# Performance work log

Measured on AMD Instinct MI355X. Metric: run time of the kernel, lower is better.

## Reference

```python
import jax, jax.numpy as jnp
import numpy as np

B, n, D, L, Hff, heads = 64, 512, 128, 3, 512, 8
N = B * n
deg = 16
E = N * deg
dh = D // heads
EPS = 1e-5


def setup_inputs() -> dict:
    key = jax.random.key(0)
    ks = jax.random.split(key, 16)
    x = jax.random.normal(ks[0], (N, D), jnp.float32)
    # within-graph random edges (TSP kNN-style), offset per graph
    src = jax.random.randint(ks[1], (B, n * deg), 0, n)
    dst = jax.random.randint(ks[2], (B, n * deg), 0, n)
    off = (jnp.arange(B) * n)[:, None]
    edge_index = jnp.stack([(src + off).reshape(-1), (dst + off).reshape(-1)]).astype(jnp.int32)
    edge_attr = jax.random.normal(ks[3], (E, D), jnp.float32)
    batch = jnp.repeat(jnp.arange(B, dtype=jnp.int32), n)
    s = 0.02
    wk = jax.random.split(ks[4], 8)
    w = lambda k, shape: jax.random.normal(k, shape, jnp.float32) * s
    return dict(
        x=x, edge_index=edge_index, edge_attr=edge_attr, batch=batch,
        Wq=w(wk[0], (L, D, D)), bq=jnp.zeros((L, D), jnp.float32),
        Wk=w(wk[1], (L, D, D)), bk=jnp.zeros((L, D), jnp.float32),
        Wv=w(wk[2], (L, D, D)), bv=jnp.zeros((L, D), jnp.float32),
        We=w(wk[3], (L, D, D)),  # lin_edge has no bias in PyG TransformerConv
        Wskip=w(wk[4], (L, D, D)), bskip=jnp.zeros((L, D), jnp.float32),
        gn_g=jnp.ones((L - 1, D), jnp.float32), gn_b=jnp.zeros((L - 1, D), jnp.float32),
        gn_a=jnp.ones((L - 1, D), jnp.float32),
        ffW1=w(wk[5], (D, Hff)), ffb1=jnp.zeros((Hff,), jnp.float32),
        fgn_g=jnp.ones((Hff,), jnp.float32), fgn_b=jnp.zeros((Hff,), jnp.float32),
        fgn_a=jnp.ones((Hff,), jnp.float32),
        ffW2=w(wk[6], (Hff, D)), ffb2=jnp.zeros((D,), jnp.float32),
    )


def _graph_norm(x, batch, gamma, beta, alpha):
    # GraphNorm: per-graph mean/var per channel, learnable mean scale alpha
    mean = jax.ops.segment_sum(x, batch, num_segments=B) / n
    xc = x - alpha * mean[batch]
    var = jax.ops.segment_sum(xc * xc, batch, num_segments=B) / n
    return gamma * xc * jax.lax.rsqrt(var[batch] + EPS) + beta


def _transformer_conv(x, src, dst, ea, Wq, bq, Wk, bk, Wv, bv, We, Ws, bs):
    q = (x @ Wq + bq).reshape(-1, heads, dh)
    k = (x @ Wk + bk).reshape(-1, heads, dh)
    v = (x @ Wv + bv).reshape(-1, heads, dh)
    e = (ea @ We).reshape(-1, heads, dh)
    ke = k[src] + e                                   # [E, h, dh]
    score = jnp.einsum('ehd,ehd->eh', q[dst], ke) / np.sqrt(dh)
    m = jax.ops.segment_max(score, dst, num_segments=N)
    ex = jnp.exp(score - m[dst])
    denom = jax.ops.segment_sum(ex, dst, num_segments=N)
    alpha = ex / denom[dst]                           # softmax over in-neighbors
    msg = alpha[..., None] * (v[src] + e)
    out = jax.ops.segment_sum(msg, dst, num_segments=N).reshape(-1, D)
    return out + x @ Ws + bs                          # root/skip connection


def reference(x, edge_index, edge_attr, batch, Wq, bq, Wk, bk, Wv, bv, We, Wskip, bskip,
              gn_g, gn_b, gn_a, ffW1, ffb1, fgn_g, fgn_b, fgn_a, ffW2, ffb2):
    src, dst = edge_index[0], edge_index[1]
    for i in range(L):
        x = _transformer_conv(x, src, dst, edge_attr, Wq[i], bq[i], Wk[i], bk[i],
                              Wv[i], bv[i], We[i], Wskip[i], bskip[i])
        if i < L - 1:
            x = _graph_norm(jax.nn.gelu(x, approximate=False), batch, gn_g[i], gn_b[i], gn_a[i])
        else:
            h = jax.nn.gelu(x @ ffW1 + ffb1, approximate=False)
            h = _graph_norm(h, batch, fgn_g, fgn_b, fgn_a)
            x = h @ ffW2 + ffb2
    node_embeddings = x.reshape(B, n, D)
    graph_feat = jax.ops.segment_sum(x, batch, num_segments=B) / n  # mean pool
    return node_embeddings, graph_feat
```

## Files before the change

### kernel.cpp

```cpp
#include <hip/hip_runtime.h>
#include <hip/hip_bf16.h>
#include <math.h>

typedef unsigned short u16;
typedef __attribute__((ext_vector_type(4))) float floatx4;
typedef __attribute__((ext_vector_type(8))) short shortx8;

#define NB 64
#define NNODE 512
#define NTOT (NB*NNODE)
#define DDIM 128
#define DEG 16
#define NEDGE (NTOT*DEG)
#define HFF 512
#define EPSV 1e-5f
#define BFRAG_U16 16384
#define EPI_LD 136

__device__ __forceinline__ float bf2f(u16 u){
  union { unsigned int i; float f; } v; v.i = ((unsigned int)u) << 16; return v.f;
}
__device__ __forceinline__ u16 f2bf(float f){
  union { float f; unsigned int i; } v; v.f = f;
  unsigned int r = v.i + 0x7FFFu + ((v.i >> 16) & 1u);
  return (u16)(r >> 16);
}
__device__ __forceinline__ float gelu_f(float x){
  return 0.5f * x * (1.0f + erff(x * 0.70710678118654752f));
}

__global__ void prep_kernel(const float* __restrict__ x, u16* __restrict__ xb,
                            int* __restrict__ counts, float* __restrict__ pool){
  int gid = blockIdx.x*256 + threadIdx.x;
  if (gid < NTOT) counts[gid] = 0;
  if (gid < NB*DDIM) pool[gid] = 0.f;
  int i = gid*4;
  float4 f = *(const float4*)(x + i);
  ushort4 o; o.x = f2bf(f.x); o.y = f2bf(f.y); o.z = f2bf(f.z); o.w = f2bf(f.w);
  *(ushort4*)(xb + i) = o;
}

__global__ void hist_kernel(const int* __restrict__ dst, int* __restrict__ counts){
  int e = blockIdx.x*256 + threadIdx.x; atomicAdd(&counts[dst[e]], 1);
}
__global__ void scan_kernel(const int* counts, int* row_ptr, int* cursor){
  __shared__ int part[1024];
  int t = threadIdx.x; int base = t*32;
  int loc[32]; int s = 0;
  #pragma unroll
  for (int i = 0; i < 32; ++i){ loc[i] = counts[base+i]; s += loc[i]; }
  part[t] = s; __syncthreads();
  for (int off = 1; off < 1024; off <<= 1){
    int v = (t >= off) ? part[t-off] : 0;
    __syncthreads(); part[t] += v; __syncthreads();
  }
  int run = part[t] - s;
  #pragma unroll
  for (int i = 0; i < 32; ++i){ row_ptr[base+i] = run; cursor[base+i] = run; run += loc[i]; }
  if (t == 0) row_ptr[NTOT] = part[1023];
}
__global__ void scatter_kernel(const int* __restrict__ src, const int* __restrict__ dst,
                               int* __restrict__ cursor, int* __restrict__ ssrc, int* __restrict__ seid){
  int e = blockIdx.x*256 + threadIdx.x;
  int d = dst[e];
  int pos = atomicAdd(&cursor[d], 1);
  ssrc[pos] = src[e]; seid[pos] = e;
}

__global__ __launch_bounds__(512, 2)
void egemm3_kernel(const float* __restrict__ ea, const int* __restrict__ seid,
                   const float* __restrict__ We, u16* __restrict__ eout, int niter){
  __shared__ u16 bfrag[3*BFRAG_U16];
  __shared__ u16 epi_s[8*16*EPI_LD];
  const int t = threadIdx.x;
  const int wave = t >> 6, lane = t & 63, quad = lane >> 4, l16 = lane & 15;
  for (int p = wave; p < 12; p += 8){
    const int l = p >> 2, kk = p & 3;
    const float* Bp = We + (size_t)l*DDIM*DDIM;
    #pragma unroll
    for (int nt = 0; nt < 8; ++nt){
      int colB = nt*16 + l16;
      shortx8 pk;
      #pragma unroll
      for (int j = 0; j < 8; ++j)
        pk[j] = (short)f2bf(Bp[(size_t)(kk*32 + quad*8 + j)*DDIM + colB]);
      *(shortx8*)&bfrag[((size_t)l*2048 + (kk*8 + nt)*64 + lane)*8] = pk;
    }
  }
  __syncthreads();
  u16* epi = &epi_s[wave*16*EPI_LD];
  for (int it = blockIdx.x; it < niter; it += gridDim.x){
    const int wrow0 = it*256 + wave*32;
    const int r0 = wrow0 + l16, r1 = r0 + 16;
    const long ar0 = (long)seid[r0], ar1 = (long)seid[r1];
    shortx8 af[2][4];
    #pragma unroll
    for (int kk = 0; kk < 4; ++kk){
      float4 x0 = *(const float4*)(ea + ar0*DDIM + kk*32 + quad*8);
      float4 x1 = *(const float4*)(ea + ar0*DDIM + kk*32 + quad*8 + 4);
      float4 y0 = *(const float4*)(ea + ar1*DDIM + kk*32 + quad*8);
      float4 y1 = *(const float4*)(ea + ar1*DDIM + kk*32 + quad*8 + 4);
      shortx8 a0, a1;
      a0[0]=(short)f2bf(x0.x); a0[1]=(short)f2bf(x0.y); a0[2]=(short)f2bf(x0.z); a0[3]=(short)f2bf(x0.w);
      a0[4]=(short)f2bf(x1.x); a0[5]=(short)f2bf(x1.y); a0[6]=(short)f2bf(x1.z); a0[7]=(short)f2bf(x1.w);
      a1[0]=(short)f2bf(y0.x); a1[1]=(short)f2bf(y0.y); a1[2]=(short)f2bf(y0.z); a1[3]=(short)f2bf(y0.w);
      a1[4]=(short)f2bf(y1.x); a1[5]=(short)f2bf(y1.y); a1[6]=(short)f2bf(y1.z); a1[7]=(short)f2bf(y1.w);
      af[0][kk] = a0; af[1][kk] = a1;
    }
    #pragma unroll
    for (int l = 0; l < 3; ++l){
      floatx4 acc[2][8] = {};
      #pragma unroll
      for (int kk = 0; kk < 4; ++kk){
        #pragma unroll
        for (int nt = 0; nt < 8; ++nt){
          shortx8 bfr = *(const shortx8*)&bfrag[((size_t)l*2048 + (kk*8 + nt)*64 + lane)*8];
          acc[0][nt] = __builtin_amdgcn_mfma_f32_16x16x32_bf16(af[0][kk], bfr, acc[0][nt], 0, 0, 0);
          acc[1][nt] = __builtin_amdgcn_mfma_f32_16x16x32_bf16(af[1][kk], bfr, acc[1][nt], 0, 0, 0);
        }
      }
      u16* o16 = eout + (size_t)l*NEDGE*DDIM;
      #pragma unroll
      for (int mt = 0; mt < 2; ++mt){
        #pragma unroll
        for (int nt = 0; nt < 8; ++nt){
          #pragma unroll
          for (int r = 0; r < 4; ++r)
            epi[(quad*4 + r)*EPI_LD + nt*16 + l16] = f2bf(acc[mt][nt][r]);
        }
        #pragma unroll
        for (int j = 0; j < 4; ++j){
          int row = j*4 + quad;
          uint4 d = *(const uint4*)&epi[row*EPI_LD + l16*8];
          *(uint4*)(o16 + (size_t)(wrow0 + mt*16 + row)*DDIM + l16*8) = d;
        }
      }
    }
  }
}

struct Gemm2Cfg {
  const float* B[4];
  const float* bias[4];
  float* o32[4];
  u16* o16[4];
  const int* a_idx;
  const float* nA;
  const float* nBp;
  int ldb, ld_out, bcolmul, ocolmul, gelu, mtiles;
};

template<bool ABF>
__global__ __launch_bounds__(256, 3)
void gemm2_kernel(const void* __restrict__ Aptr, Gemm2Cfg cfg){
  __shared__ u16 lds[BFRAG_U16 + 4*16*EPI_LD];
  const int t = threadIdx.x;
  const int wave = t >> 6, lane = t & 63, quad = lane >> 4, l16 = lane & 15;
  const int cb = blockIdx.y;
  const float* Bp = cfg.B[cb];
  const int col0b = cb * cfg.bcolmul;
  {
    const int kk = wave;
    #pragma unroll
    for (int nt = 0; nt < 8; ++nt){
      int colB = col0b + nt*16 + l16;
      shortx8 pk;
      #pragma unroll
      for (int j = 0; j < 8; ++j)
        pk[j] = (short)f2bf(Bp[(size_t)(kk*32 + quad*8 + j)*cfg.ldb + colB]);
      *(shortx8*)&lds[((kk*8 + nt)*64 + lane)*8] = pk;
    }
  }
  __syncthreads();
  const float* biasp = cfg.bias[cb];
  const int col0o = cb * cfg.ocolmul;
  float bias_r[8];
  #pragma unroll
  for (int nt = 0; nt < 8; ++nt)
    bias_r[nt] = biasp ? biasp[col0o + nt*16 + l16] : 0.0f;
  u16* epi = &lds[BFRAG_U16 + wave*16*EPI_LD];

  for (int tile = blockIdx.x; tile < cfg.mtiles; tile += gridDim.x){
    const int wrow0 = tile*128 + wave*32;
    const int r0 = wrow0 + l16, r1 = wrow0 + 16 + l16;
    const long ar0 = cfg.a_idx ? (long)cfg.a_idx[r0] : (long)r0;
    const long ar1 = cfg.a_idx ? (long)cfg.a_idx[r1] : (long)r1;
    shortx8 af[2][4];
    if (ABF){
      const u16* Ab = (const u16*)Aptr;
      #pragma unroll
      for (int kk = 0; kk < 4; ++kk){
        af[0][kk] = *(const shortx8*)(Ab + ar0*128 + kk*32 + quad*8);
        af[1][kk] = *(const shortx8*)(Ab + ar1*128 + kk*32 + quad*8);
      }
    } else {
      const float* Af = (const float*)Aptr;
      const int g = wrow0 >> 9;
      #pragma unroll
      for (int kk = 0; kk < 4; ++kk){
        float4 x0 = *(const float4*)(Af + ar0*128 + kk*32 + quad*8);
        float4 x1 = *(const float4*)(Af + ar0*128 + kk*32 + quad*8 + 4);
        float4 y0 = *(const float4*)(Af + ar1*128 + kk*32 + quad*8);
        float4 y1 = *(const float4*)(Af + ar1*128 + kk*32 + quad*8 + 4);
        if (cfg.nA){
          const float4 A0 = *(const float4*)(cfg.nA  + (size_t)g*DDIM + kk*32 + quad*8);
          const float4 A1 = *(const float4*)(cfg.nA  + (size_t)g*DDIM + kk*32 + quad*8 + 4);
          const float4 B0 = *(const float4*)(cfg.nBp + (size_t)g*DDIM + kk*32 + quad*8);
          const float4 B1 = *(const float4*)(cfg.nBp + (size_t)g*DDIM + kk*32 + quad*8 + 4);
          x0.x = gelu_f(x0.x)*A0.x + B0.x; x0.y = gelu_f(x0.y)*A0.y + B0.y;
          x0.z = gelu_f(x0.z)*A0.z + B0.z; x0.w = gelu_f(x0.w)*A0.w + B0.w;
          x1.x = gelu_f(x1.x)*A1.x + B1.x; x1.y = gelu_f(x1.y)*A1.y + B1.y;
          x1.z = gelu_f(x1.z)*A1.z + B1.z; x1.w = gelu_f(x1.w)*A1.w + B1.w;
          y0.x = gelu_f(y0.x)*A0.x + B0.x; y0.y = gelu_f(y0.y)*A0.y + B0.y;
          y0.z = gelu_f(y0.z)*A0.z + B0.z; y0.w = gelu_f(y0.w)*A0.w + B0.w;
          y1.x = gelu_f(y1.x)*A1.x + B1.x; y1.y = gelu_f(y1.y)*A1.y + B1.y;
          y1.z = gelu_f(y1.z)*A1.z + B1.z; y1.w = gelu_f(y1.w)*A1.w + B1.w;
        }
        shortx8 a0, a1;
        a0[0]=(short)f2bf(x0.x); a0[1]=(short)f2bf(x0.y); a0[2]=(short)f2bf(x0.z); a0[3]=(short)f2bf(x0.w);
        a0[4]=(short)f2bf(x1.x); a0[5]=(short)f2bf(x1.y); a0[6]=(short)f2bf(x1.z); a0[7]=(short)f2bf(x1.w);
        a1[0]=(short)f2bf(y0.x); a1[1]=(short)f2bf(y0.y); a1[2]=(short)f2bf(y0.z); a1[3]=(short)f2bf(y0.w);
        a1[4]=(short)f2bf(y1.x); a1[5]=(short)f2bf(y1.y); a1[6]=(short)f2bf(y1.z); a1[7]=(short)f2bf(y1.w);
        af[0][kk] = a0; af[1][kk] = a1;
      }
    }
    floatx4 acc[2][8] = {};
    #pragma unroll
    for (int kk = 0; kk < 4; ++kk){
      #pragma unroll
      for (int nt = 0; nt < 8; ++nt){
        shortx8 bfr = *(const shortx8*)&lds[((kk*8 + nt)*64 + lane)*8];
        acc[0][nt] = __builtin_amdgcn_mfma_f32_16x16x32_bf16(af[0][kk], bfr, acc[0][nt], 0, 0, 0);
        acc[1][nt] = __builtin_amdgcn_mfma_f32_16x16x32_bf16(af[1][kk], bfr, acc[1][nt], 0, 0, 0);
      }
    }
    u16* o16 = cfg.o16[cb];
    if (o16){
      #pragma unroll
      for (int mt = 0; mt < 2; ++mt){
        #pragma unroll
        for (int nt = 0; nt < 8; ++nt){
          #pragma unroll
          for (int r = 0; r < 4; ++r){
            float v = acc[mt][nt][r] + bias_r[nt];
            if (cfg.gelu) v = gelu_f(v);
            epi[(quad*4 + r)*EPI_LD + nt*16 + l16] = f2bf(v);
          }
        }
        #pragma unroll
        for (int j = 0; j < 4; ++j){
          int row = j*4 + quad;
          uint4 d = *(const uint4*)&epi[row*EPI_LD + l16*8];
          *(uint4*)(o16 + (size_t)(wrow0 + mt*16 + row)*cfg.ld_out + col0o + l16*8) = d;
        }
      }
    } else {
      float* o32 = cfg.o32[cb];
      #pragma unroll
      for (int nt = 0; nt < 8; ++nt){
        #pragma unroll
        for (int mt = 0; mt < 2; ++mt){
          #pragma unroll
          for (int r = 0; r < 4; ++r){
            int row = wrow0 + mt*16 + quad*4 + r;
            float v = acc[mt][nt][r] + bias_r[nt];
            if (cfg.gelu) v = gelu_f(v);
            o32[(size_t)row*cfg.ld_out + col0o + nt*16 + l16] = v;
          }
        }
      }
    }
  }
}

struct GemmCfg {
  const float* B[4];
  const float* bias[4];
  float* o32[4];
  u16* o16[4];
  float* pool;
  const float* nA;
  const float* nBp;
  int ldb, ld_out, K, bcolmul, ocolmul, gelu;
};

__global__ __launch_bounds__(256, 2)
void gemm_old(const u16* __restrict__ Ab, GemmCfg cfg){
  __shared__ u16 As[128][136];
  __shared__ u16 Bs[128][136];
  const int t = threadIdx.x;
  const int wave = t >> 6, lane = t & 63, quad = lane >> 4, l16 = lane & 15;
  const int row0 = blockIdx.x * 128;
  const int cb = blockIdx.y;
  const float* Bp = cfg.B[cb];
  const int col0b = cb * cfg.bcolmul;
  const int K = cfg.K;
  const int g = row0 >> 9;
  floatx4 acc[2][8] = {};
  for (int kc = 0; kc < K; kc += 128){
    #pragma unroll
    for (int j = 0; j < 8; ++j){
      int idx8 = t + j*256;
      int elem = idx8 << 3;
      int r = elem >> 7, c = elem & 127;
      uint4 d = *(const uint4*)(Ab + (size_t)(row0+r)*K + kc + c);
      if (cfg.nA){
        const float4 A0 = *(const float4*)(cfg.nA  + (size_t)g*K + kc + c);
        const float4 A1 = *(const float4*)(cfg.nA  + (size_t)g*K + kc + c + 4);
        const float4 B0 = *(const float4*)(cfg.nBp + (size_t)g*K + kc + c);
        const float4 B1 = *(const float4*)(cfg.nBp + (size_t)g*K + kc + c + 4);
        u16* pu = (u16*)&d;
        pu[0] = f2bf(bf2f(pu[0])*A0.x + B0.x);
        pu[1] = f2bf(bf2f(pu[1])*A0.y + B0.y);
        pu[2] = f2bf(bf2f(pu[2])*A0.z + B0.z);
        pu[3] = f2bf(bf2f(pu[3])*A0.w + B0.w);
        pu[4] = f2bf(bf2f(pu[4])*A1.x + B1.x);
        pu[5] = f2bf(bf2f(pu[5])*A1.y + B1.y);
        pu[6] = f2bf(bf2f(pu[6])*A1.z + B1.z);
        pu[7] = f2bf(bf2f(pu[7])*A1.w + B1.w);
      }
      *(uint4*)&As[r][c] = d;
    }
    #pragma unroll
    for (int j = 0; j < 16; ++j){
      int gi = t + j*256;
      int c = gi & 127;
      int k4 = (gi >> 7) << 2;
      size_t boff = (size_t)(kc + k4)*cfg.ldb + col0b + c;
      float f0 = Bp[boff];
      float f1 = Bp[boff + cfg.ldb];
      float f2 = Bp[boff + 2*(size_t)cfg.ldb];
      float f3 = Bp[boff + 3*(size_t)cfg.ldb];
      u16* wp = &Bs[c][k4];
      wp[0]=f2bf(f0); wp[1]=f2bf(f1); wp[2]=f2bf(f2); wp[3]=f2bf(f3);
    }
    __syncthreads();
    const int wm0 = wave*32;
    #pragma unroll
    for (int kk = 0; kk < 4; ++kk){
      shortx8 a0 = *(const shortx8*)&As[wm0 + l16][kk*32 + quad*8];
      shortx8 a1 = *(const shortx8*)&As[wm0 + 16 + l16][kk*32 + quad*8];
      #pragma unroll
      for (int nt = 0; nt < 8; ++nt){
        shortx8 bfr = *(const shortx8*)&Bs[nt*16 + l16][kk*32 + quad*8];
        acc[0][nt] = __builtin_amdgcn_mfma_f32_16x16x32_bf16(a0, bfr, acc[0][nt], 0, 0, 0);
        acc[1][nt] = __builtin_amdgcn_mfma_f32_16x16x32_bf16(a1, bfr, acc[1][nt], 0, 0, 0);
      }
    }
    __syncthreads();
  }
  const float* biasp = cfg.bias[cb];
  float* o32 = cfg.o32[cb];
  const int col0o = cb * cfg.ocolmul;
  const int wm0 = wave*32;
  float* psum = (float*)As;
  if (cfg.pool){
    __syncthreads();
    if (t < 128) psum[t] = 0.f;
    __syncthreads();
  }
  #pragma unroll
  for (int nt = 0; nt < 8; ++nt){
    int col = col0o + nt*16 + l16;
    float bvv = biasp ? biasp[col] : 0.0f;
    float cs = 0.f;
    #pragma unroll
    for (int mt = 0; mt < 2; ++mt){
      #pragma unroll
      for (int r = 0; r < 4; ++r){
        int row = row0 + wm0 + mt*16 + quad*4 + r;
        float v = acc[mt][nt][r] + bvv;
        if (cfg.gelu) v = gelu_f(v);
        o32[(size_t)row * cfg.ld_out + col] = v;
        cs += v;
      }
    }
    if (cfg.pool) atomicAdd(&psum[nt*16 + l16], cs);
  }
  if (cfg.pool){
    __syncthreads();
    if (t < 128) atomicAdd(&cfg.pool[(row0 >> 9)*DDIM + t], psum[t] * (1.0f/NNODE));
  }
}

__global__ __launch_bounds__(256)
void attn_kernel(const int* __restrict__ row_ptr, const int* __restrict__ ssrc,
                 const u16* __restrict__ e_rows,
                 const u16* __restrict__ qb, const u16* __restrict__ kb, const u16* __restrict__ vb,
                 const float* __restrict__ skip, float* __restrict__ y){
  int b = blockIdx.x;
  int xcd = b & 7, i = b >> 3;
  int g = xcd*8 + (i >> 7), slot = i & 127;
  int wave = threadIdx.x >> 6, lane = threadIdx.x & 63;
  int dst = g*NNODE + slot*4 + wave;
  const int ch = lane*2;
  ushort2 qp = *(const ushort2*)(qb + (size_t)dst*DDIM + ch);
  float q0 = bf2f(qp.x), q1 = bf2f(qp.y);
  int beg = row_ptr[dst], end = row_ptr[dst+1];
  float mh = -INFINITY, lh = 0.f, a0 = 0.f, a1 = 0.f;
  if (beg < end){
    int s = ssrc[beg];
    ushort2 ep = *(const ushort2*)(e_rows + (size_t)beg*DDIM + ch);
    ushort2 kp = *(const ushort2*)(kb + (size_t)s*DDIM + ch);
    ushort2 vp = *(const ushort2*)(vb + (size_t)s*DDIM + ch);
    for (int idx = beg; idx < end; ++idx){
      int nx = idx + 1;
      ushort2 epn = ep, kpn = kp, vpn = vp;
      if (nx < end){
        int sn = ssrc[nx];
        epn = *(const ushort2*)(e_rows + (size_t)nx*DDIM + ch);
        kpn = *(const ushort2*)(kb + (size_t)sn*DDIM + ch);
        vpn = *(const ushort2*)(vb + (size_t)sn*DDIM + ch);
      }
      float e0 = bf2f(ep.x), e1 = bf2f(ep.y);
      float p = q0*(bf2f(kp.x)+e0) + q1*(bf2f(kp.y)+e1);
      p += __shfl_xor(p, 1);
      p += __shfl_xor(p, 2);
      p += __shfl_xor(p, 4);
      float sc = p * 0.25f;
      float mn = fmaxf(mh, sc);
      float cs = __expf(mh - mn), w = __expf(sc - mn);
      lh = lh*cs + w;
      a0 = a0*cs + w*(bf2f(vp.x)+e0);
      a1 = a1*cs + w*(bf2f(vp.y)+e1);
      mh = mn;
      ep = epn; kp = kpn; vp = vpn;
    }
  }
  float r = lh > 0.f ? 1.0f/lh : 0.f;
  float2 sp = *(const float2*)(skip + (size_t)dst*DDIM + ch);
  float2 o; o.x = a0*r + sp.x; o.y = a1*r + sp.y;
  *(float2*)(y + (size_t)dst*DDIM + ch) = o;
}

__global__ __launch_bounds__(128)
void gstats_part(const float* __restrict__ y, float* __restrict__ ps, float* __restrict__ pq){
  int b = blockIdx.x, g = b >> 3, chunk = b & 7, c = threadIdx.x;
  const float* base = y + (size_t)g*NNODE*DDIM + (size_t)chunk*64*DDIM;
  float s = 0.f, q = 0.f;
  for (int i = 0; i < 64; ++i){
    float v = gelu_f(base[(size_t)i*DDIM + c]);
    s += v; q += v*v;
  }
  ps[b*DDIM + c] = s; pq[b*DDIM + c] = q;
}
__global__ __launch_bounds__(128)
void gstats_comb(const float* __restrict__ ps, const float* __restrict__ pq,
                 const float* __restrict__ gamma, const float* __restrict__ beta,
                 const float* __restrict__ alpha, float* __restrict__ nA, float* __restrict__ nB){
  int g = blockIdx.x, c = threadIdx.x;
  float s = 0.f, q = 0.f;
  #pragma unroll
  for (int j = 0; j < 8; ++j){ s += ps[(g*8+j)*DDIM + c]; q += pq[(g*8+j)*DDIM + c]; }
  float mean = s * (1.f/NNODE);
  float msq  = q * (1.f/NNODE);
  float a = alpha[c];
  float invv = rsqrtf(msq - mean*mean*a*(2.f-a) + EPSV);
  float ga = gamma[c]*invv;
  nA[g*DDIM + c] = ga;
  nB[g*DDIM + c] = beta[c] - ga*a*mean;
}

__global__ __launch_bounds__(512)
void fstats_part(const u16* __restrict__ gb, float* __restrict__ ps, float* __restrict__ pq){
  int b = blockIdx.x, g = b >> 3, chunk = b & 7, c = threadIdx.x;
  const u16* base = gb + (size_t)g*NNODE*HFF + (size_t)chunk*64*HFF;
  float s = 0.f, q = 0.f;
  for (int i = 0; i < 64; ++i){
    float v = bf2f(base[(size_t)i*HFF + c]);
    s += v; q += v*v;
  }
  ps[b*HFF + c] = s; pq[b*HFF + c] = q;
}
__global__ __launch_bounds__(512)
void fstats_comb(const float* __restrict__ ps, const float* __restrict__ pq,
                 const float* __restrict__ gamma, const float* __restrict__ beta,
                 const float* __restrict__ alpha, float* __restrict__ nA, float* __restrict__ nB){
  int g = blockIdx.x, c = threadIdx.x;
  float s = 0.f, q = 0.f;
  #pragma unroll
  for (int j = 0; j < 8; ++j){ s += ps[(g*8+j)*HFF + c]; q += pq[(g*8+j)*HFF + c]; }
  float mean = s * (1.f/NNODE);
  float msq  = q * (1.f/NNODE);
  float a = alpha[c];
  float invv = rsqrtf(msq - mean*mean*a*(2.f-a) + EPSV);
  float ga = gamma[c]*invv;
  nA[g*HFF + c] = ga;
  nB[g*HFF + c] = beta[c] - ga*a*mean;
}

extern "C" void kernel_launch(void* const* d_in, const int* in_sizes, int n_in,
                              void* d_out, int out_size, void* d_ws, size_t ws_size,
                              hipStream_t stream){
  const float* x_in = (const float*)d_in[0];
  const int*   eidx = (const int*)d_in[1];
  const float* ea   = (const float*)d_in[2];
  const float* Wq   = (const float*)d_in[4];
  const float* bq   = (const float*)d_in[5];
  const float* Wk   = (const float*)d_in[6];
  const float* bk   = (const float*)d_in[7];
  const float* Wv   = (const float*)d_in[8];
  const float* bv   = (const float*)d_in[9];
  const float* We   = (const float*)d_in[10];
  const float* Wsk  = (const float*)d_in[11];
  const float* bsk  = (const float*)d_in[12];
  const float* gn_g = (const float*)d_in[13];
  const float* gn_b = (const float*)d_in[14];
  const float* gn_a = (const float*)d_in[15];
  const float* ffW1 = (const float*)d_in[16];
  const float* ffb1 = (const float*)d_in[17];
  const float* fgn_g= (const float*)d_in[18];
  const float* fgn_b= (const float*)d_in[19];
  const float* fgn_a= (const float*)d_in[20];
  const float* ffW2 = (const float*)d_in[21];
  const float* ffb2 = (const float*)d_in[22];
  const int* srcA = eidx;
  const int* dstA = eidx + NEDGE;

  char* w = (char*)d_ws;
  auto alloc = [&](size_t bytes)->char*{ char* p = w; w += (bytes + 255) & ~(size_t)255; return p; };
  int* counts  = (int*)alloc((size_t)NTOT*4);
  int* row_ptr = (int*)alloc((size_t)(NTOT+1)*4);
  int* ssrc    = (int*)alloc((size_t)NEDGE*4);
  int* seid    = (int*)alloc((size_t)NEDGE*4);
  u16* e_bf    = (u16*)alloc((size_t)3*NEDGE*DDIM*2);
  u16* x_bf    = (u16*)alloc((size_t)NTOT*DDIM*2);
  u16* qb      = (u16*)alloc((size_t)NTOT*DDIM*2);
  u16* kb      = (u16*)alloc((size_t)NTOT*DDIM*2);
  u16* vb      = (u16*)alloc((size_t)NTOT*DDIM*2);
  float* skipb = (float*)alloc((size_t)NTOT*DDIM*4);
  float* yb    = (float*)alloc((size_t)NTOT*DDIM*4);
  float* nAb   = (float*)alloc((size_t)NB*HFF*4);
  float* nBb   = (float*)alloc((size_t)NB*HFF*4);
  float* psbuf = (float*)alloc((size_t)NB*8*HFF*4);
  float* pqbuf = (float*)alloc((size_t)NB*8*HFF*4);
  u16* g_bf  = e_bf;
  float* pool = (float*)d_out + (size_t)NTOT*DDIM;

  prep_kernel<<<NTOT*DDIM/1024, 256, 0, stream>>>(x_in, x_bf, counts, pool);
  hist_kernel<<<NEDGE/256, 256, 0, stream>>>(dstA, counts);
  scan_kernel<<<1, 1024, 0, stream>>>(counts, row_ptr, counts);
  scatter_kernel<<<NEDGE/256, 256, 0, stream>>>(srcA, dstA, counts, ssrc, seid);

  egemm3_kernel<<<512, 512, 0, stream>>>(ea, seid, We, e_bf, NEDGE/256);

  for (int l = 0; l < 3; ++l){
    Gemm2Cfg cq = {};
    cq.B[0]=Wq + (size_t)l*DDIM*DDIM; cq.B[1]=Wk + (size_t)l*DDIM*DDIM;
    cq.B[2]=Wv + (size_t)l*DDIM*DDIM; cq.B[3]=Wsk + (size_t)l*DDIM*DDIM;
    cq.bias[0]=bq + l*DDIM; cq.bias[1]=bk + l*DDIM; cq.bias[2]=bv + l*DDIM; cq.bias[3]=bsk + l*DDIM;
    cq.o16[0]=qb; cq.o16[1]=kb; cq.o16[2]=vb; cq.o16[3]=nullptr;
    cq.o32[3]=skipb;
    cq.ldb = DDIM; cq.ld_out = DDIM; cq.bcolmul = 0; cq.ocolmul = 0; cq.gelu = 0;
    cq.mtiles = NTOT/128;
    if (l == 0){
      gemm2_kernel<true><<<dim3(NTOT/128, 4), 256, 0, stream>>>(x_bf, cq);
    } else {
      cq.nA = nAb; cq.nBp = nBb;
      gemm2_kernel<false><<<dim3(NTOT/128, 4), 256, 0, stream>>>(yb, cq);
    }

    attn_kernel<<<NTOT/4, 256, 0, stream>>>(row_ptr, ssrc,
        e_bf + (size_t)l*NEDGE*DDIM, qb, kb, vb, skipb, yb);

    if (l < 2){
      gstats_part<<<NB*8, 128, 0, stream>>>(yb, psbuf, pqbuf);
      gstats_comb<<<NB, 128, 0, stream>>>(psbuf, pqbuf,
          gn_g + l*DDIM, gn_b + l*DDIM, gn_a + l*DDIM, nAb, nBb);
    }
  }

  Gemm2Cfg c1 = {};
  for (int i2 = 0; i2 < 4; ++i2){ c1.B[i2] = ffW1; c1.bias[i2] = ffb1; c1.o16[i2] = g_bf; }
  c1.ldb = HFF; c1.ld_out = HFF; c1.bcolmul = 128; c1.ocolmul = 128; c1.gelu = 1;
  c1.mtiles = NTOT/128;
  gemm2_kernel<false><<<dim3(NTOT/128, 4), 256, 0, stream>>>(yb, c1);

  fstats_part<<<NB*8, 512, 0, stream>>>(g_bf, psbuf, pqbuf);
  fstats_comb<<<NB, 512, 0, stream>>>(psbuf, pqbuf, fgn_g, fgn_b, fgn_a, nAb, nBb);

  GemmCfg c2 = {};
  for (int i2 = 0; i2 < 4; ++i2){ c2.B[i2] = ffW2; c2.bias[i2] = ffb2; c2.o32[i2] = (float*)d_out; }
  c2.ldb = DDIM; c2.ld_out = DDIM; c2.K = HFF; c2.bcolmul = 0; c2.ocolmul = 0; c2.gelu = 0;
  c2.pool = pool;
  c2.nA = nAb; c2.nBp = nBb;
  gemm_old<<<dim3(NTOT/128, 1), 256, 0, stream>>>(g_bf, c2);
}
```

Before: 1.066 ms.

## Store attention output as bf16 with fused GELU, prefetch edge tiles, split softmax chains

The attention kernel now applies GELU itself and writes bf16 into x_bf instead of fp32 into a separate buffer. GraphNorm stats and the next layer's QKV GEMM read this bf16 tensor, and the GEMM applies the norm affine in bf16. This halves the traffic for the intermediate node features and drops a buffer. The edge GEMM now prefetches the next tile's edge attributes into registers and launches half as many blocks. The attention loop splits the online softmax into two independent chains merged at the end, which adds ILP. The main risk is the extra rounding from storing post-GELU activations in bf16.

Result: faster. 939.6 us (-11.8%).

```diff
diff --git a/kernel.cpp b/kernel.cpp
--- a/kernel.cpp
+++ b/kernel.cpp
@@ -89,23 +89,43 @@
   }
   __syncthreads();
   u16* epi = &epi_s[wave*16*EPI_LD];
-  for (int it = blockIdx.x; it < niter; it += gridDim.x){
+  float4 pf[16];
+  int it = blockIdx.x;
+  if (it < niter){
+    const int w0 = it*256 + wave*32;
+    const long br0 = (long)seid[w0 + l16], br1 = (long)seid[w0 + 16 + l16];
+    #pragma unroll
+    for (int kk = 0; kk < 4; ++kk){
+      pf[kk*4+0] = *(const float4*)(ea + br0*DDIM + kk*32 + quad*8);
+      pf[kk*4+1] = *(const float4*)(ea + br0*DDIM + kk*32 + quad*8 + 4);
+      pf[kk*4+2] = *(const float4*)(ea + br1*DDIM + kk*32 + quad*8);
+      pf[kk*4+3] = *(const float4*)(ea + br1*DDIM + kk*32 + quad*8 + 4);
+    }
+  }
+  while (it < niter){
     const int wrow0 = it*256 + wave*32;
-    const int r0 = wrow0 + l16, r1 = r0 + 16;
-    const long ar0 = (long)seid[r0], ar1 = (long)seid[r1];
+    const int nxt = it + gridDim.x;
     shortx8 af[2][4];
     #pragma unroll
     for (int kk = 0; kk < 4; ++kk){
-      float4 x0 = *(const float4*)(ea + ar0*DDIM + kk*32 + quad*8);
-      float4 x1 = *(const float4*)(ea + ar0*DDIM + kk*32 + quad*8 + 4);
-      float4 y0 = *(const float4*)(ea + ar1*DDIM + kk*32 + quad*8);
-      float4 y1 = *(const float4*)(ea + ar1*DDIM + kk*32 + quad*8 + 4);
+      float4 x0 = pf[kk*4+0], x1 = pf[kk*4+1], y0 = pf[kk*4+2], y1 = pf[kk*4+3];
       shortx8 a0, a1;
       a0[0]=(short)f2bf(x0.x); a0[1]=(short)f2bf(x0.y); a0[2]=(short)f2bf(x0.z); a0[3]=(short)f2bf(x0.w);
       a0[4]=(short)f2bf(x1.x); a0[5]=(short)f2bf(x1.y); a0[6]=(short)f2bf(x1.z); a0[7]=(short)f2bf(x1.w);
       a1[0]=(short)f2bf(y0.x); a1[1]=(short)f2bf(y0.y); a1[2]=(short)f2bf(y0.z); a1[3]=(short)f2bf(y0.w);
       a1[4]=(short)f2bf(y1.x); a1[5]=(short)f2bf(y1.y); a1[6]=(short)f2bf(y1.z); a1[7]=(short)f2bf(y1.w);
       af[0][kk] = a0; af[1][kk] = a1;
+    }
+    if (nxt < niter){
+      const int w2 = nxt*256 + wave*32;
+      const long br0 = (long)seid[w2 + l16], br1 = (long)seid[w2 + 16 + l16];
+      #pragma unroll
+      for (int kk = 0; kk < 4; ++kk){
+        pf[kk*4+0] = *(const float4*)(ea + br0*DDIM + kk*32 + quad*8);
+        pf[kk*4+1] = *(const float4*)(ea + br0*DDIM + kk*32 + quad*8 + 4);
+        pf[kk*4+2] = *(const float4*)(ea + br1*DDIM + kk*32 + quad*8);
+        pf[kk*4+3] = *(const float4*)(ea + br1*DDIM + kk*32 + quad*8 + 4);
+      }
     }
     #pragma unroll
     for (int l = 0; l < 3; ++l){
@@ -136,6 +156,7 @@
         }
       }
     }
+    it = nxt;
   }
 }
 
@@ -144,15 +165,14 @@
   const float* bias[4];
   float* o32[4];
   u16* o16[4];
-  const int* a_idx;
   const float* nA;
   const float* nBp;
   int ldb, ld_out, bcolmul, ocolmul, gelu, mtiles;
 };
 
-template<bool ABF>
+template<bool AFF>
 __global__ __launch_bounds__(256, 3)
-void gemm2_kernel(const void* __restrict__ Aptr, Gemm2Cfg cfg){
+void gemm2_kernel(const u16* __restrict__ Ab, Gemm2Cfg cfg){
   __shared__ u16 lds[BFRAG_U16 + 4*16*EPI_LD];
   const int t = threadIdx.x;
   const int wave = t >> 6, lane = t & 63, quad = lane >> 4, l16 = lane & 15;
@@ -182,47 +202,29 @@
 
   for (int tile = blockIdx.x; tile < cfg.mtiles; tile += gridDim.x){
     const int wrow0 = tile*128 + wave*32;
-    const int r0 = wrow0 + l16, r1 = wrow0 + 16 + l16;
-    const long ar0 = cfg.a_idx ? (long)cfg.a_idx[r0] : (long)r0;
-    const long ar1 = cfg.a_idx ? (long)cfg.a_idx[r1] : (long)r1;
+    const int r0 = wrow0 + l16, r1 = r0 + 16;
+    const int g = wrow0 >> 9;
     shortx8 af[2][4];
-    if (ABF){
-      const u16* Ab = (const u16*)Aptr;
-      #pragma unroll
-      for (int kk = 0; kk < 4; ++kk){
-        af[0][kk] = *(const shortx8*)(Ab + ar0*128 + kk*32 + quad*8);
-        af[1][kk] = *(const shortx8*)(Ab + ar1*128 + kk*32 + quad*8);
-      }
-    } else {
-      const float* Af = (const float*)Aptr;
-      const int g = wrow0 >> 9;
-      #pragma unroll
-      for (int kk = 0; kk < 4; ++kk){
-        float4 x0 = *(const float4*)(Af + ar0*128 + kk*32 + quad*8);
-        float4 x1 = *(const float4*)(Af + ar0*128 + kk*32 + quad*8 + 4);
-        float4 y0 = *(const float4*)(Af + ar1*128 + kk*32 + quad*8);
-        float4 y1 = *(const float4*)(Af + ar1*128 + kk*32 + quad*8 + 4);
-        if (cfg.nA){
-          const float4 A0 = *(const float4*)(cfg.nA  + (size_t)g*DDIM + kk*32 + quad*8);
-          const float4 A1 = *(const float4*)(cfg.nA  + (size_t)g*DDIM + kk*32 + quad*8 + 4);
-          const float4 B0 = *(const float4*)(cfg.nBp + (size_t)g*DDIM + kk*32 + quad*8);
-          const float4 B1 = *(const float4*)(cfg.nBp + (size_t)g*DDIM + kk*32 + quad*8 + 4);
-          x0.x = gelu_f(x0.x)*A0.x + B0.x; x0.y = gelu_f(x0.y)*A0.y + B0.y;
-          x0.z = gelu_f(x0.z)*A0.z + B0.z; x0.w = gelu_f(x0.w)*A0.w + B0.w;
-          x1.x = gelu_f(x1.x)*A1.x + B1.x; x1.y = gelu_f(x1.y)*A1.y + B1.y;
-          x1.z = gelu_f(x1.z)*A1.z + B1.z; x1.w = gelu_f(x1.w)*A1.w + B1.w;
-          y0.x = gelu_f(y0.x)*A0.x + B0.x; y0.y = gelu_f(y0.y)*A0.y + B0.y;
-          y0.z = gelu_f(y0.z)*A0.z + B0.z; y0.w = gelu_f(y0.w)*A0.w + B0.w;
-          y1.x = gelu_f(y1.x)*A1.x + B1.x; y1.y = gelu_f(y1.y)*A1.y + B1.y;
-          y1.z = gelu_f(y1.z)*A1.z + B1.z; y1.w = gelu_f(y1.w)*A1.w + B1.w;
-        }
-        shortx8 a0, a1;
-        a0[0]=(short)f2bf(x0.x); a0[1]=(short)f2bf(x0.y); a0[2]=(short)f2bf(x0.z); a0[3]=(short)f2bf(x0.w);
-        a0[4]=(short)f2bf(x1.x); a0[5]=(short)f2bf(x1.y); a0[6]=(short)f2bf(x1.z); a0[7]=(short)f2bf(x1.w);
-        a1[0]=(short)f2bf(y0.x); a1[1]=(short)f2bf(y0.y); a1[2]=(short)f2bf(y0.z); a1[3]=(short)f2bf(y0.w);
-        a1[4]=(short)f2bf(y1.x); a1[5]=(short)f2bf(y1.y); a1[6]=(short)f2bf(y1.z); a1[7]=(short)f2bf(y1.w);
-        af[0][kk] = a0; af[1][kk] = a1;
-      }
+    #pragma unroll
+    for (int kk = 0; kk < 4; ++kk){
+      shortx8 a0 = *(const shortx8*)(Ab + (size_t)r0*128 + kk*32 + quad*8);
+      shortx8 a1 = *(const shortx8*)(Ab + (size_t)r1*128 + kk*32 + quad*8);
+      if (AFF){
+        const float4 A0 = *(const float4*)(cfg.nA  + (size_t)g*DDIM + kk*32 + quad*8);
+        const float4 A1 = *(const float4*)(cfg.nA  + (size_t)g*DDIM + kk*32 + quad*8 + 4);
+        const float4 B0 = *(const float4*)(cfg.nBp + (size_t)g*DDIM + kk*32 + quad*8);
+        const float4 B1 = *(const float4*)(cfg.nBp + (size_t)g*DDIM + kk*32 + quad*8 + 4);
+        u16* p0 = (u16*)&a0; u16* p1 = (u16*)&a1;
+        p0[0]=f2bf(bf2f(p0[0])*A0.x+B0.x); p0[1]=f2bf(bf2f(p0[1])*A0.y+B0.y);
+        p0[2]=f2bf(bf2f(p0[2])*A0.z+B0.z); p0[3]=f2bf(bf2f(p0[3])*A0.w+B0.w);
+        p0[4]=f2bf(bf2f(p0[4])*A1.x+B1.x); p0[5]=f2bf(bf2f(p0[5])*A1.y+B1.y);
+        p0[6]=f2bf(bf2f(p0[6])*A1.z+B1.z); p0[7]=f2bf(bf2f(p0[7])*A1.w+B1.w);
+        p1[0]=f2bf(bf2f(p1[0])*A0.x+B0.x); p1[1]=f2bf(bf2f(p1[1])*A0.y+B0.y);
+        p1[2]=f2bf(bf2f(p1[2])*A0.z+B0.z); p1[3]=f2bf(bf2f(p1[3])*A0.w+B0.w);
+        p1[4]=f2bf(bf2f(p1[4])*A1.x+B1.x); p1[5]=f2bf(bf2f(p1[5])*A1.y+B1.y);
+        p1[6]=f2bf(bf2f(p1[6])*A1.z+B1.z); p1[7]=f2bf(bf2f(p1[7])*A1.w+B1.w);
+      }
+      af[0][kk] = a0; af[1][kk] = a1;
     }
     floatx4 acc[2][8] = {};
     #pragma unroll
@@ -383,11 +385,12 @@
   }
 }
 
+template<int GELU_OUT>
 __global__ __launch_bounds__(256)
 void attn_kernel(const int* __restrict__ row_ptr, const int* __restrict__ ssrc,
                  const u16* __restrict__ e_rows,
                  const u16* __restrict__ qb, const u16* __restrict__ kb, const u16* __restrict__ vb,
-                 const float* __restrict__ skip, float* __restrict__ y){
+                 const float* __restrict__ skip, u16* __restrict__ yout){
   int b = blockIdx.x;
   int xcd = b & 7, i = b >> 3;
   int g = xcd*8 + (i >> 7), slot = i & 127;
@@ -397,49 +400,79 @@
   ushort2 qp = *(const ushort2*)(qb + (size_t)dst*DDIM + ch);
   float q0 = bf2f(qp.x), q1 = bf2f(qp.y);
   int beg = row_ptr[dst], end = row_ptr[dst+1];
-  float mh = -INFINITY, lh = 0.f, a0 = 0.f, a1 = 0.f;
-  if (beg < end){
-    int s = ssrc[beg];
-    ushort2 ep = *(const ushort2*)(e_rows + (size_t)beg*DDIM + ch);
-    ushort2 kp = *(const ushort2*)(kb + (size_t)s*DDIM + ch);
-    ushort2 vp = *(const ushort2*)(vb + (size_t)s*DDIM + ch);
-    for (int idx = beg; idx < end; ++idx){
-      int nx = idx + 1;
-      ushort2 epn = ep, kpn = kp, vpn = vp;
-      if (nx < end){
-        int sn = ssrc[nx];
-        epn = *(const ushort2*)(e_rows + (size_t)nx*DDIM + ch);
-        kpn = *(const ushort2*)(kb + (size_t)sn*DDIM + ch);
-        vpn = *(const ushort2*)(vb + (size_t)sn*DDIM + ch);
-      }
-      float e0 = bf2f(ep.x), e1 = bf2f(ep.y);
-      float p = q0*(bf2f(kp.x)+e0) + q1*(bf2f(kp.y)+e1);
-      p += __shfl_xor(p, 1);
-      p += __shfl_xor(p, 2);
-      p += __shfl_xor(p, 4);
+  float mA = -INFINITY, lA = 0.f, y0A = 0.f, y1A = 0.f;
+  float mB = -INFINITY, lB = 0.f, y0B = 0.f, y1B = 0.f;
+  int idx = beg;
+  for (; idx + 1 < end; idx += 2){
+    int s0 = ssrc[idx], s1 = ssrc[idx+1];
+    ushort2 e0p = *(const ushort2*)(e_rows + (size_t)idx*DDIM + ch);
+    ushort2 e1p = *(const ushort2*)(e_rows + (size_t)(idx+1)*DDIM + ch);
+    ushort2 k0p = *(const ushort2*)(kb + (size_t)s0*DDIM + ch);
+    ushort2 k1p = *(const ushort2*)(kb + (size_t)s1*DDIM + ch);
+    ushort2 v0p = *(const ushort2*)(vb + (size_t)s0*DDIM + ch);
+    ushort2 v1p = *(const ushort2*)(vb + (size_t)s1*DDIM + ch);
+    {
+      float e0 = bf2f(e0p.x), e1 = bf2f(e0p.y);
+      float p = q0*(bf2f(k0p.x)+e0) + q1*(bf2f(k0p.y)+e1);
+      p += __shfl_xor(p, 1); p += __shfl_xor(p, 2); p += __shfl_xor(p, 4);
       float sc = p * 0.25f;
-      float mn = fmaxf(mh, sc);
-      float cs = __expf(mh - mn), w = __expf(sc - mn);
-      lh = lh*cs + w;
-      a0 = a0*cs + w*(bf2f(vp.x)+e0);
-      a1 = a1*cs + w*(bf2f(vp.y)+e1);
-      mh = mn;
-      ep = epn; kp = kpn; vp = vpn;
-    }
-  }
+      float mn = fmaxf(mA, sc);
+      float cs = __expf(mA - mn), w = __expf(sc - mn);
+      lA = lA*cs + w;
+      y0A = y0A*cs + w*(bf2f(v0p.x)+e0);
+      y1A = y1A*cs + w*(bf2f(v0p.y)+e1);
+      mA = mn;
+    }
+    {
+      float e0 = bf2f(e1p.x), e1 = bf2f(e1p.y);
+      float p = q0*(bf2f(k1p.x)+e0) + q1*(bf2f(k1p.y)+e1);
+      p += __shfl_xor(p, 1); p += __shfl_xor(p, 2); p += __shfl_xor(p, 4);
+      float sc = p * 0.25f;
+      float mn = fmaxf(mB, sc);
+      float cs = __expf(mB - mn), w = __expf(sc - mn);
+      lB = lB*cs + w;
+      y0B = y0B*cs + w*(bf2f(v1p.x)+e0);
+      y1B = y1B*cs + w*(bf2f(v1p.y)+e1);
+      mB = mn;
+    }
+  }
+  if (idx < end){
+    int s0 = ssrc[idx];
+    ushort2 e0p = *(const ushort2*)(e_rows + (size_t)idx*DDIM + ch);
+    ushort2 k0p = *(const ushort2*)(kb + (size_t)s0*DDIM + ch);
+    ushort2 v0p = *(const ushort2*)(vb + (size_t)s0*DDIM + ch);
+    float e0 = bf2f(e0p.x), e1 = bf2f(e0p.y);
+    float p = q0*(bf2f(k0p.x)+e0) + q1*(bf2f(k0p.y)+e1);
+    p += __shfl_xor(p, 1); p += __shfl_xor(p, 2); p += __shfl_xor(p, 4);
+    float sc = p * 0.25f;
+    float mn = fmaxf(mA, sc);
+    float cs = __expf(mA - mn), w = __expf(sc - mn);
+    lA = lA*cs + w;
+    y0A = y0A*cs + w*(bf2f(v0p.x)+e0);
+    y1A = y1A*cs + w*(bf2f(v0p.y)+e1);
+    mA = mn;
+  }
+  float mn = fmaxf(mA, mB);
+  float cA = lA > 0.f ? __expf(mA - mn) : 0.f;
+  float cB = lB > 0.f ? __expf(mB - mn) : 0.f;
+  float lh = lA*cA + lB*cB;
+  float a0 = y0A*cA + y0B*cB;
+  float a1 = y1A*cA + y1B*cB;
   float r = lh > 0.f ? 1.0f/lh : 0.f;
   float2 sp = *(const float2*)(skip + (size_t)dst*DDIM + ch);
-  float2 o; o.x = a0*r + sp.x; o.y = a1*r + sp.y;
-  *(float2*)(y + (size_t)dst*DDIM + ch) = o;
+  float o0 = a0*r + sp.x, o1 = a1*r + sp.y;
+  if (GELU_OUT){ o0 = gelu_f(o0); o1 = gelu_f(o1); }
+  ushort2 ov; ov.x = f2bf(o0); ov.y = f2bf(o1);
+  *(ushort2*)(yout + (size_t)dst*DDIM + ch) = ov;
 }
 
 __global__ __launch_bounds__(128)
-void gstats_part(const float* __restrict__ y, float* __restrict__ ps, float* __restrict__ pq){
+void gstats_part(const u16* __restrict__ gy, float* __restrict__ ps, float* __restrict__ pq){
   int b = blockIdx.x, g = b >> 3, chunk = b & 7, c = threadIdx.x;
-  const float* base = y + (size_t)g*NNODE*DDIM + (size_t)chunk*64*DDIM;
+  const u16* base = gy + (size_t)g*NNODE*DDIM + (size_t)chunk*64*DDIM;
   float s = 0.f, q = 0.f;
   for (int i = 0; i < 64; ++i){
-    float v = gelu_f(base[(size_t)i*DDIM + c]);
+    float v = bf2f(base[(size_t)i*DDIM + c]);
     s += v; q += v*v;
   }
   ps[b*DDIM + c] = s; pq[b*DDIM + c] = q;
@@ -529,7 +562,6 @@
   u16* kb      = (u16*)alloc((size_t)NTOT*DDIM*2);
   u16* vb      = (u16*)alloc((size_t)NTOT*DDIM*2);
   float* skipb = (float*)alloc((size_t)NTOT*DDIM*4);
-  float* yb    = (float*)alloc((size_t)NTOT*DDIM*4);
   float* nAb   = (float*)alloc((size_t)NB*HFF*4);
   float* nBb   = (float*)alloc((size_t)NB*HFF*4);
   float* psbuf = (float*)alloc((size_t)NB*8*HFF*4);
@@ -542,7 +574,7 @@
   scan_kernel<<<1, 1024, 0, stream>>>(counts, row_ptr, counts);
   scatter_kernel<<<NEDGE/256, 256, 0, stream>>>(srcA, dstA, counts, ssrc, seid);
 
-  egemm3_kernel<<<512, 512, 0, stream>>>(ea, seid, We, e_bf, NEDGE/256);
+  egemm3_kernel<<<256, 512, 0, stream>>>(ea, seid, We, e_bf, NEDGE/256);
 
   for (int l = 0; l < 3; ++l){
     Gemm2Cfg cq = {};
@@ -554,19 +586,21 @@
     cq.ldb = DDIM; cq.ld_out = DDIM; cq.bcolmul = 0; cq.ocolmul = 0; cq.gelu = 0;
     cq.mtiles = NTOT/128;
     if (l == 0){
-      gemm2_kernel<true><<<dim3(NTOT/128, 4), 256, 0, stream>>>(x_bf, cq);
+      gemm2_kernel<false><<<dim3(NTOT/128, 4), 256, 0, stream>>>(x_bf, cq);
     } else {
       cq.nA = nAb; cq.nBp = nBb;
-      gemm2_kernel<false><<<dim3(NTOT/128, 4), 256, 0, stream>>>(yb, cq);
-    }
-
-    attn_kernel<<<NTOT/4, 256, 0, stream>>>(row_ptr, ssrc,
-        e_bf + (size_t)l*NEDGE*DDIM, qb, kb, vb, skipb, yb);
+      gemm2_kernel<true><<<dim3(NTOT/128, 4), 256, 0, stream>>>(x_bf, cq);
+    }
 
     if (l < 2){
-      gstats_part<<<NB*8, 128, 0, stream>>>(yb, psbuf, pqbuf);
+      attn_kernel<1><<<NTOT/4, 256, 0, stream>>>(row_ptr, ssrc,
+          e_bf + (size_t)l*NEDGE*DDIM, qb, kb, vb, skipb, x_bf);
+      gstats_part<<<NB*8, 128, 0, stream>>>(x_bf, psbuf, pqbuf);
       gstats_comb<<<NB, 128, 0, stream>>>(psbuf, pqbuf,
           gn_g + l*DDIM, gn_b + l*DDIM, gn_a + l*DDIM, nAb, nBb);
+    } else {
+      attn_kernel<0><<<NTOT/4, 256, 0, stream>>>(row_ptr, ssrc,
+          e_bf + (size_t)l*NEDGE*DDIM, qb, kb, vb, skipb, x_bf);
     }
   }
 
@@ -574,7 +608,7 @@
   for (int i2 = 0; i2 < 4; ++i2){ c1.B[i2] = ffW1; c1.bias[i2] = ffb1; c1.o16[i2] = g_bf; }
   c1.ldb = HFF; c1.ld_out = HFF; c1.bcolmul = 128; c1.ocolmul = 128; c1.gelu = 1;
   c1.mtiles = NTOT/128;
-  gemm2_kernel<false><<<dim3(NTOT/128, 4), 256, 0, stream>>>(yb, c1);
+  gemm2_kernel<false><<<dim3(NTOT/128, 4), 256, 0, stream>>>(x_bf, c1);
 
   fstats_part<<<NB*8, 512, 0, stream>>>(g_bf, psbuf, pqbuf);
   fstats_comb<<<NB, 512, 0, stream>>>(psbuf, pqbuf, fgn_g, fgn_b, fgn_a, nAb, nBb);
```
